# Performance work log

Hardware: AMD Instinct MI355X
Metric: run time of the kernel (lower is better)

The kernel has to match this reference:

```python
import jax, jax.numpy as jnp
import numpy as np

EMB_W, COMMIT_W, ENT_W = 1.0, 0.25, 0.1  # loss weights from init_kwargs


def setup_inputs() -> dict:
    key = jax.random.key(0)
    k1, k2 = jax.random.split(key)
    B, H, W, D, K = 32, 32, 32, 64, 1024
    inputs = jax.random.normal(k1, (B, H, W, D), dtype=jnp.float32)
    # keras RandomUniform default: U(-0.05, 0.05)
    codebook = jax.random.uniform(k2, (K, D), dtype=jnp.float32, minval=-0.05, maxval=0.05)
    return {"inputs": inputs, "codebook": codebook}


def reference(inputs, codebook):
    # inputs: [B,H,W,D], codebook: [K,D]
    D = inputs.shape[-1]
    x = inputs.reshape(-1, D)  # [N,D]
    dist = (
        jnp.sum(x * x, axis=-1, keepdims=True)
        - 2.0 * (x @ codebook.T)
        + jnp.sum(codebook * codebook, axis=-1)
    )  # [N,K]
    tokens = jnp.argmin(dist, axis=-1)  # [N]
    emb = codebook[tokens].reshape(inputs.shape)  # [B,H,W,D]

    embedding_loss = EMB_W * jnp.mean((jax.lax.stop_gradient(emb) - inputs) ** 2)
    commitment_loss = COMMIT_W * jnp.mean((emb - jax.lax.stop_gradient(inputs)) ** 2)
    # 'entropy' loss as written in call(): mean over codebook of per-code min distance
    entropy_loss = ENT_W * jnp.mean(jnp.min(dist, axis=0))
    loss = embedding_loss + commitment_loss + entropy_loss

    # training=True path: straight-through estimator
    out = inputs + jax.lax.stop_gradient(emb - inputs)
    return out, loss
```

## Files before the change

kernel.cpp:

```cpp
#include <hip/hip_runtime.h>
#include <math.h>

#define NROWS 32768
#define NCODE 1024
#define AMB_CAP 8192
#define GAP_THRESH 1.5e-4f

typedef __attribute__((ext_vector_type(8))) short bf16x8;
typedef __attribute__((ext_vector_type(4))) float f32x4;

__device__ __forceinline__ unsigned short bf16_rne(float f) {
    unsigned u = __float_as_uint(f);
    unsigned r = u + 0x7FFFu + ((u >> 16) & 1u);
    return (unsigned short)(r >> 16);
}

typedef const __attribute__((address_space(1))) unsigned GU;
typedef __attribute__((address_space(3))) unsigned LU;
__device__ __forceinline__ void gl_lds16(const void* g, void* l) {
    __builtin_amdgcn_global_load_lds((GU*)g, (LU*)l, 16, 0, 0);
}
__device__ __forceinline__ void gl_lds4(const void* g, void* l) {
    __builtin_amdgcn_global_load_lds((GU*)g, (LU*)l, 4, 0, 0);
}

__global__ __launch_bounds__(64) void vq_prep(
    const float* __restrict__ cb, float* __restrict__ cn4,
    unsigned* __restrict__ minK, unsigned* __restrict__ counter,
    float* __restrict__ gsumsq, unsigned* __restrict__ ticket,
    unsigned short* __restrict__ wsB)
{
    int c = blockIdx.x * 64 + threadIdx.x;
    if (c == 0) { *counter = 0u; *gsumsq = 0.f; *ticket = 0u; }
    float v[64];
    const float4* src = (const float4*)(cb + (size_t)c * 64);
    float s = 0.f;
    #pragma unroll
    for (int i = 0; i < 16; i++) {
        float4 t = src[i];
        v[i*4+0] = t.x; v[i*4+1] = t.y; v[i*4+2] = t.z; v[i*4+3] = t.w;
        s += t.x*t.x + t.y*t.y + t.z*t.z + t.w*t.w;
    }
    cn4[c] = s + 4.0f;
    minK[c] = 0x7F800000u;
    int cc = c >> 6, ct = (c >> 4) & 3, cl = c & 15;
    #pragma unroll
    for (int q = 0; q < 4; q++) {
        int half = q & 1, lo = q >> 1;
        #pragma unroll
        for (int g = 0; g < 4; g++) {
            unsigned short u8[8] __attribute__((aligned(16)));
            #pragma unroll
            for (int j = 0; j < 8; j++) {
                float f = v[half*32 + g*8 + j];
                unsigned short h = bf16_rne(f);
                if (lo) h = bf16_rne(f - __uint_as_float((unsigned)h << 16));
                u8[j] = h;
            }
            size_t off = (size_t)cc * 8192 + ct * 2048 + q * 512 + (g * 16 + cl) * 8;
            *(uint4*)(wsB + off) = *(const uint4*)u8;
        }
    }
}

__global__ __launch_bounds__(512, 4) void vq_main(
    const float* __restrict__ x, const float* __restrict__ cb,
    const unsigned short* __restrict__ wsB, const float* __restrict__ cn4,
    float* __restrict__ out, unsigned* __restrict__ minK,
    unsigned* __restrict__ counter, int* __restrict__ amb,
    float* __restrict__ gsumsq)
{
    __shared__ __align__(16) unsigned char Bb[2][16384];
    __shared__ float cn4L[2][64];
    __shared__ unsigned scrE[1024];
    __shared__ float mD1[128], mD2[128];
    __shared__ int   mI1[128];
    __shared__ int   tokS[64];
    __shared__ float redS[8];

    const int tid = threadIdx.x;
    const int lane = tid & 63;
    const int wi = tid >> 6;
    const int g = wi >> 1;
    const int h = wi & 1;
    const int ln15 = lane & 15;
    const int q = lane >> 4;
    const int row0 = blockIdx.x * 64;
    const int rot = blockIdx.x & 15;

    #pragma unroll
    for (int jj = 0; jj < 2; jj++) scrE[jj*512 + tid] = 0x7F800000u;

    const char* wsBb = (const char*)wsB;
    {
        int wbase = (tid & ~63) * 16;
        gl_lds16(wsBb + rot*16384 +        tid*16, (void*)&Bb[0][wbase]);
        gl_lds16(wsBb + rot*16384 + 8192 + tid*16, (void*)&Bb[0][8192 + wbase]);
        if (wi == 0) gl_lds4(cn4 + rot*64 + lane, (void*)&cn4L[0][0]);
    }

    bf16x8 Ah0, Ah1, Al0, Al1;
    float xnm4[4];
    {
        const float* xr = x + (size_t)(row0 + g*16 + ln15) * 64 + q * 8;
        float4 f0 = *(const float4*)xr;
        float4 f1 = *(const float4*)(xr + 4);
        float4 f2 = *(const float4*)(xr + 32);
        float4 f3 = *(const float4*)(xr + 36);
        float fa[8] = {f0.x,f0.y,f0.z,f0.w,f1.x,f1.y,f1.z,f1.w};
        float fb[8] = {f2.x,f2.y,f2.z,f2.w,f3.x,f3.y,f3.z,f3.w};
        unsigned short hh8[8] __attribute__((aligned(16)));
        unsigned short ll8[8] __attribute__((aligned(16)));
        unsigned short h28[8] __attribute__((aligned(16)));
        unsigned short l28[8] __attribute__((aligned(16)));
        float ss = 0.f;
        #pragma unroll
        for (int j = 0; j < 8; j++) {
            ss += fa[j]*fa[j] + fb[j]*fb[j];
            unsigned short hh = bf16_rne(fa[j]);
            hh8[j] = hh; ll8[j] = bf16_rne(fa[j] - __uint_as_float((unsigned)hh << 16));
            hh = bf16_rne(fb[j]);
            h28[j] = hh; l28[j] = bf16_rne(fb[j] - __uint_as_float((unsigned)hh << 16));
        }
        Ah0 = *(const bf16x8*)hh8; Al0 = *(const bf16x8*)ll8;
        Ah1 = *(const bf16x8*)h28; Al1 = *(const bf16x8*)l28;
        ss += __shfl_xor(ss, 16);
        ss += __shfl_xor(ss, 32);
        #pragma unroll
        for (int r = 0; r < 4; r++)
            xnm4[r] = __shfl(ss, (q << 2) | r, 64) - 4.0f;
    }

    float d1[4], d2[4];
    int   i1[4];
    #pragma unroll
    for (int r = 0; r < 4; r++) { d1[r] = INFINITY; d2[r] = INFINITY; i1[r] = 0; }

    for (int s = 0; s < 16; s++) {
        __syncthreads();
        const int cb_ = s & 1, nb = (s + 1) & 1;
        const int cphys = (s + rot) & 15;
        if (s < 15) {
            const int cnx = (s + 1 + rot) & 15;
            int wbase = (tid & ~63) * 16;
            gl_lds16(wsBb + cnx*16384 +        tid*16, (void*)&Bb[nb][wbase]);
            gl_lds16(wsBb + cnx*16384 + 8192 + tid*16, (void*)&Bb[nb][8192 + wbase]);
            if (wi == 0) gl_lds4(cn4 + cnx*64 + lane, (void*)&cn4L[nb][0]);
        }
        const unsigned char* buf = Bb[cb_];
        #pragma unroll
        for (int lct = 0; lct < 2; lct++) {
            const int ct = 2*h + lct;
            bf16x8 Bh0 = *(const bf16x8*)(buf + ct*4096 +    0 + lane*16);
            bf16x8 Bh1 = *(const bf16x8*)(buf + ct*4096 + 1024 + lane*16);
            bf16x8 Bl0 = *(const bf16x8*)(buf + ct*4096 + 2048 + lane*16);
            bf16x8 Bl1 = *(const bf16x8*)(buf + ct*4096 + 3072 + lane*16);
            float cn4v = cn4L[cb_][ct*16 + ln15];
            int kid = cphys*64 + ct*16 + ln15;
            f32x4 acc = {0.f, 0.f, 0.f, 0.f};
            acc = __builtin_amdgcn_mfma_f32_16x16x32_bf16(Ah0, Bh0, acc, 0, 0, 0);
            acc = __builtin_amdgcn_mfma_f32_16x16x32_bf16(Ah1, Bh1, acc, 0, 0, 0);
            acc = __builtin_amdgcn_mfma_f32_16x16x32_bf16(Ah0, Bl0, acc, 0, 0, 0);
            acc = __builtin_amdgcn_mfma_f32_16x16x32_bf16(Ah1, Bl1, acc, 0, 0, 0);
            acc = __builtin_amdgcn_mfma_f32_16x16x32_bf16(Al0, Bh0, acc, 0, 0, 0);
            acc = __builtin_amdgcn_mfma_f32_16x16x32_bf16(Al1, Bh1, acc, 0, 0, 0);
            float cminv = INFINITY;
            #pragma unroll
            for (int r = 0; r < 4; r++) {
                float wv = fmaf(acc[r], -2.0f, cn4v);
                bool lt = wv < d1[r];
                d2[r] = lt ? d1[r] : fminf(d2[r], wv);
                i1[r] = lt ? kid   : i1[r];
                d1[r] = lt ? wv    : d1[r];
                cminv = fminf(cminv, wv + xnm4[r]);
            }
            cminv = fminf(cminv, __shfl_xor(cminv, 16));
            cminv = fminf(cminv, __shfl_xor(cminv, 32));
            if (q == lct) atomicMin(&scrE[kid], __float_as_uint(cminv));
        }
    }
    __syncthreads();

    #pragma unroll
    for (int d = 1; d < 16; d <<= 1) {
        #pragma unroll
        for (int r = 0; r < 4; r++) {
            float od1 = __shfl_xor(d1[r], d);
            int   oi1 = __shfl_xor(i1[r], d);
            float od2 = __shfl_xor(d2[r], d);
            bool take = (od1 < d1[r]) || (od1 == d1[r] && oi1 < i1[r]);
            float loser = take ? d1[r] : od1;
            d2[r] = fminf(fminf(d2[r], od2), loser);
            d1[r] = take ? od1 : d1[r];
            i1[r] = take ? oi1 : i1[r];
        }
    }
    if (ln15 == 0) {
        #pragma unroll
        for (int r = 0; r < 4; r++) {
            int idx = (g*16 + q*4 + r) * 2 + h;
            mD1[idx] = d1[r]; mI1[idx] = i1[r]; mD2[idx] = d2[r];
        }
    }
    __syncthreads();

    if (tid < 64) {
        float a1 = mD1[tid*2],   b1 = mD1[tid*2+1];
        int   ai = mI1[tid*2],   bi = mI1[tid*2+1];
        float a2 = mD2[tid*2],   b2 = mD2[tid*2+1];
        bool ta = (a1 < b1) || (a1 == b1 && ai < bi);
        float D1 = ta ? a1 : b1;
        int   I1 = ta ? ai : bi;
        float D2 = ta ? fminf(a2, b1) : fminf(b2, a1);
        tokS[tid] = I1;
        if (D2 - D1 < GAP_THRESH) {
            unsigned idx = atomicAdd(counter, 1u);
            if (idx < AMB_CAP) { amb[2*idx] = row0 + tid; amb[2*idx+1] = I1; }
        }
    }

    #pragma unroll
    for (int jj = 0; jj < 2; jj++) {
        int c = jj*512 + tid;
        unsigned u = scrE[c];
        if (u < minK[c]) atomicMin(&minK[c], u);
    }
    __syncthreads();

    {
        float acc2 = 0.f;
        #pragma unroll
        for (int uu = 0; uu < 2; uu++) {
            int u = uu*512 + tid;
            int row = u >> 4, c4 = u & 15;
            int tok = tokS[row];
            float4 c = ((const float4*)(cb + (size_t)tok*64))[c4];
            float4 xx = ((const float4*)(x + (size_t)(row0 + row)*64))[c4];
            ((float4*)(out + (size_t)(row0 + row)*64))[c4] = c;
            float dx = c.x-xx.x, dy = c.y-xx.y, dz = c.z-xx.z, dw = c.w-xx.w;
            acc2 += dx*dx + dy*dy + dz*dz + dw*dw;
        }
        #pragma unroll
        for (int o = 32; o > 0; o >>= 1) acc2 += __shfl_down(acc2, o);
        if (lane == 0) redS[wi] = acc2;
        __syncthreads();
        if (tid == 0) {
            float t = 0.f;
            #pragma unroll
            for (int w = 0; w < 8; w++) t += redS[w];
            atomicAdd(gsumsq, t);
        }
    }
}

__global__ __launch_bounds__(256) void vq_tail(
    const float* __restrict__ x, const float* __restrict__ cb,
    float* __restrict__ out, const unsigned* __restrict__ counter,
    const int* __restrict__ amb, float* __restrict__ gsumsq,
    unsigned* __restrict__ ticket, const unsigned* __restrict__ minK,
    float* __restrict__ out_loss)
{
    __shared__ double xs[64];
    __shared__ double bd[256];
    __shared__ int    bi[256];
    __shared__ unsigned lastS;
    __shared__ float redS[4];

    const int tid = threadIdx.x;

    unsigned cnt = *counter; if (cnt > AMB_CAP) cnt = AMB_CAP;
    for (unsigned i = blockIdx.x; i < cnt; i += gridDim.x) {
        int row = amb[2*i], oldk = amb[2*i+1];
        __syncthreads();
        if (tid < 64) xs[tid] = (double)x[(size_t)row*64 + tid];
        __syncthreads();
        double xn = 0.0;
        #pragma unroll 8
        for (int d = 0; d < 64; d++) xn += xs[d]*xs[d];
        double best = INFINITY; int bk = 1 << 30;
        #pragma unroll
        for (int j = 0; j < 4; j++) {
            int k = j*256 + tid;
            const float4* c4 = (const float4*)(cb + (size_t)k*64);
            double dot = 0.0, cn2 = 0.0;
            #pragma unroll
            for (int t = 0; t < 16; t++) {
                float4 cv = c4[t];
                double cx = (double)cv.x, cy = (double)cv.y, cz = (double)cv.z, cw = (double)cv.w;
                dot += xs[t*4+0]*cx + xs[t*4+1]*cy + xs[t*4+2]*cz + xs[t*4+3]*cw;
                cn2 += cx*cx + cy*cy + cz*cz + cw*cw;
            }
            double dist = (xn - 2.0*dot) + cn2;
            if (dist < best || (dist == best && k < bk)) { best = dist; bk = k; }
        }
        bd[tid] = best; bi[tid] = bk;
        __syncthreads();
        for (int s = 128; s > 0; s >>= 1) {
            if (tid < s) {
                double od = bd[tid+s]; int ok = bi[tid+s];
                if (od < bd[tid] || (od == bd[tid] && ok < bi[tid])) { bd[tid] = od; bi[tid] = ok; }
            }
            __syncthreads();
        }
        int bestk = bi[0];
        if (bestk != oldk) {
            double part = 0.0;
            if (tid < 64) {
                float cn = cb[(size_t)bestk*64 + tid];
                float co = cb[(size_t)oldk*64 + tid];
                out[(size_t)row*64 + tid] = cn;
                double dn = (double)cn - xs[tid];
                double dl = (double)co - xs[tid];
                part = dn*dn - dl*dl;
            }
            __syncthreads();
            bd[tid] = part;
            __syncthreads();
            for (int s = 128; s > 0; s >>= 1) {
                if (tid < s) bd[tid] += bd[tid+s];
                __syncthreads();
            }
            if (tid == 0) atomicAdd(gsumsq, (float)bd[0]);
        }
    }

    __syncthreads();
    if (tid == 0) {
        __threadfence();
        lastS = (atomicAdd(ticket, 1u) == (unsigned)(gridDim.x - 1)) ? 1u : 0u;
    }
    __syncthreads();
    if (lastS) {
        __threadfence();
        float s = 0.f;
        #pragma unroll
        for (int jj = 0; jj < 4; jj++)
            s += __uint_as_float(minK[jj*256 + tid]);
        #pragma unroll
        for (int o = 32; o > 0; o >>= 1) s += __shfl_down(s, o);
        if ((tid & 63) == 0) redS[tid >> 6] = s;
        __syncthreads();
        if (tid == 0) {
            float gs = atomicAdd(gsumsq, 0.0f);
            float tot = redS[0] + redS[1] + redS[2] + redS[3];
            out_loss[0] = 1.25f * (gs / 2097152.0f) + 0.1f * (tot / 1024.0f);
        }
    }
}

extern "C" void kernel_launch(void* const* d_in, const int* in_sizes, int n_in,
                              void* d_out, int out_size, void* d_ws, size_t ws_size,
                              hipStream_t stream) {
    const float* x  = (const float*)d_in[0];
    const float* cb = (const float*)d_in[1];
    float* out = (float*)d_out;

    char* ws = (char*)d_ws;
    unsigned*       counter = (unsigned*)ws;
    float*          gsumsq  = (float*)(ws + 4);
    unsigned*       ticket  = (unsigned*)(ws + 8);
    float*          cn4     = (float*)(ws + 1024);
    unsigned*       minK    = (unsigned*)(ws + 8192);
    int*            amb     = (int*)(ws + 16384);
    unsigned short* wsB     = (unsigned short*)(ws + 131072);

    vq_prep<<<16,  64,  0, stream>>>(cb, cn4, minK, counter, gsumsq, ticket, wsB);
    vq_main<<<512, 512, 0, stream>>>(x, cb, wsB, cn4, out, minK, counter, amb, gsumsq);
    vq_tail<<<64,  256, 0, stream>>>(x, cb, out, counter, amb, gsumsq, ticket, minK,
                                     out + 2097152);
}
```

Baseline: 130.6 us.

## Halve rows per block, give each wave one code tile, split MFMA chains

Each block now handles 32 rows instead of 64, and each of the 8 waves takes a single 16-code tile in place of two. This doubles the grid to 1024 blocks and raises the occupancy hint to 8 blocks. The six dependent MFMAs are split into two independent accumulator chains that are summed afterwards, shortening the dependency chain. In exchange, every block still streams the whole codebook through LDS, so total codebook traffic and per-block minK atomics double. The final argmin merge now reduces across 4 code quarters.

```diff
diff --git a/kernel.cpp b/kernel.cpp
--- a/kernel.cpp
+++ b/kernel.cpp
@@ -63,7 +63,7 @@
     }
 }
 
-__global__ __launch_bounds__(512, 4) void vq_main(
+__global__ __launch_bounds__(512, 8) void vq_main(
     const float* __restrict__ x, const float* __restrict__ cb,
     const unsigned short* __restrict__ wsB, const float* __restrict__ cn4,
     float* __restrict__ out, unsigned* __restrict__ minK,
@@ -75,21 +75,21 @@
     __shared__ unsigned scrE[1024];
     __shared__ float mD1[128], mD2[128];
     __shared__ int   mI1[128];
-    __shared__ int   tokS[64];
+    __shared__ int   tokS[32];
     __shared__ float redS[8];
 
     const int tid = threadIdx.x;
     const int lane = tid & 63;
     const int wi = tid >> 6;
-    const int g = wi >> 1;
-    const int h = wi & 1;
+    const int g = wi >> 2;
+    const int cq = wi & 3;
     const int ln15 = lane & 15;
     const int q = lane >> 4;
-    const int row0 = blockIdx.x * 64;
+    const int row0 = blockIdx.x * 32;
     const int rot = blockIdx.x & 15;
 
-    #pragma unroll
-    for (int jj = 0; jj < 2; jj++) scrE[jj*512 + tid] = 0x7F800000u;
+    scrE[tid] = 0x7F800000u;
+    scrE[512 + tid] = 0x7F800000u;
 
     const char* wsBb = (const char*)wsB;
     {
@@ -148,26 +148,26 @@
             if (wi == 0) gl_lds4(cn4 + cnx*64 + lane, (void*)&cn4L[nb][0]);
         }
         const unsigned char* buf = Bb[cb_];
-        #pragma unroll
-        for (int lct = 0; lct < 2; lct++) {
-            const int ct = 2*h + lct;
+        {
+            const int ct = cq;
             bf16x8 Bh0 = *(const bf16x8*)(buf + ct*4096 +    0 + lane*16);
             bf16x8 Bh1 = *(const bf16x8*)(buf + ct*4096 + 1024 + lane*16);
             bf16x8 Bl0 = *(const bf16x8*)(buf + ct*4096 + 2048 + lane*16);
             bf16x8 Bl1 = *(const bf16x8*)(buf + ct*4096 + 3072 + lane*16);
             float cn4v = cn4L[cb_][ct*16 + ln15];
             int kid = cphys*64 + ct*16 + ln15;
-            f32x4 acc = {0.f, 0.f, 0.f, 0.f};
-            acc = __builtin_amdgcn_mfma_f32_16x16x32_bf16(Ah0, Bh0, acc, 0, 0, 0);
-            acc = __builtin_amdgcn_mfma_f32_16x16x32_bf16(Ah1, Bh1, acc, 0, 0, 0);
-            acc = __builtin_amdgcn_mfma_f32_16x16x32_bf16(Ah0, Bl0, acc, 0, 0, 0);
-            acc = __builtin_amdgcn_mfma_f32_16x16x32_bf16(Ah1, Bl1, acc, 0, 0, 0);
-            acc = __builtin_amdgcn_mfma_f32_16x16x32_bf16(Al0, Bh0, acc, 0, 0, 0);
-            acc = __builtin_amdgcn_mfma_f32_16x16x32_bf16(Al1, Bh1, acc, 0, 0, 0);
+            f32x4 z = {0.f, 0.f, 0.f, 0.f};
+            f32x4 acc0 = __builtin_amdgcn_mfma_f32_16x16x32_bf16(Ah0, Bh0, z, 0, 0, 0);
+            f32x4 acc1 = __builtin_amdgcn_mfma_f32_16x16x32_bf16(Ah1, Bh1, z, 0, 0, 0);
+            acc0 = __builtin_amdgcn_mfma_f32_16x16x32_bf16(Ah0, Bl0, acc0, 0, 0, 0);
+            acc1 = __builtin_amdgcn_mfma_f32_16x16x32_bf16(Ah1, Bl1, acc1, 0, 0, 0);
+            acc0 = __builtin_amdgcn_mfma_f32_16x16x32_bf16(Al0, Bh0, acc0, 0, 0, 0);
+            acc1 = __builtin_amdgcn_mfma_f32_16x16x32_bf16(Al1, Bh1, acc1, 0, 0, 0);
             float cminv = INFINITY;
             #pragma unroll
             for (int r = 0; r < 4; r++) {
-                float wv = fmaf(acc[r], -2.0f, cn4v);
+                float sdot = acc0[r] + acc1[r];
+                float wv = fmaf(sdot, -2.0f, cn4v);
                 bool lt = wv < d1[r];
                 d2[r] = lt ? d1[r] : fminf(d2[r], wv);
                 i1[r] = lt ? kid   : i1[r];
@@ -176,7 +176,7 @@
             }
             cminv = fminf(cminv, __shfl_xor(cminv, 16));
             cminv = fminf(cminv, __shfl_xor(cminv, 32));
-            if (q == lct) atomicMin(&scrE[kid], __float_as_uint(cminv));
+            if (q == 0) atomicMin(&scrE[kid], __float_as_uint(cminv));
         }
     }
     __syncthreads();
@@ -198,20 +198,23 @@
     if (ln15 == 0) {
         #pragma unroll
         for (int r = 0; r < 4; r++) {
-            int idx = (g*16 + q*4 + r) * 2 + h;
+            int idx = (g*16 + q*4 + r) * 4 + cq;
             mD1[idx] = d1[r]; mI1[idx] = i1[r]; mD2[idx] = d2[r];
         }
     }
     __syncthreads();
 
-    if (tid < 64) {
-        float a1 = mD1[tid*2],   b1 = mD1[tid*2+1];
-        int   ai = mI1[tid*2],   bi = mI1[tid*2+1];
-        float a2 = mD2[tid*2],   b2 = mD2[tid*2+1];
-        bool ta = (a1 < b1) || (a1 == b1 && ai < bi);
-        float D1 = ta ? a1 : b1;
-        int   I1 = ta ? ai : bi;
-        float D2 = ta ? fminf(a2, b1) : fminf(b2, a1);
+    if (tid < 32) {
+        float D1 = mD1[tid*4], D2 = mD2[tid*4];
+        int   I1 = mI1[tid*4];
+        #pragma unroll
+        for (int c = 1; c < 4; c++) {
+            float b1 = mD1[tid*4+c], b2 = mD2[tid*4+c];
+            int   bi = mI1[tid*4+c];
+            bool tb = (b1 < D1) || (b1 == D1 && bi < I1);
+            if (tb) { D2 = fminf(D1, b2); D1 = b1; I1 = bi; }
+            else    { D2 = fminf(D2, b1); }
+        }
         tokS[tid] = I1;
         if (D2 - D1 < GAP_THRESH) {
             unsigned idx = atomicAdd(counter, 1u);
@@ -219,27 +222,22 @@
         }
     }
 
-    #pragma unroll
-    for (int jj = 0; jj < 2; jj++) {
-        int c = jj*512 + tid;
-        unsigned u = scrE[c];
-        if (u < minK[c]) atomicMin(&minK[c], u);
-    }
-    __syncthreads();
-
     {
-        float acc2 = 0.f;
-        #pragma unroll
-        for (int uu = 0; uu < 2; uu++) {
-            int u = uu*512 + tid;
-            int row = u >> 4, c4 = u & 15;
-            int tok = tokS[row];
-            float4 c = ((const float4*)(cb + (size_t)tok*64))[c4];
-            float4 xx = ((const float4*)(x + (size_t)(row0 + row)*64))[c4];
-            ((float4*)(out + (size_t)(row0 + row)*64))[c4] = c;
-            float dx = c.x-xx.x, dy = c.y-xx.y, dz = c.z-xx.z, dw = c.w-xx.w;
-            acc2 += dx*dx + dy*dy + dz*dz + dw*dw;
-        }
+        unsigned u0 = scrE[tid];
+        if (u0 < minK[tid]) atomicMin(&minK[tid], u0);
+        unsigned u1 = scrE[512 + tid];
+        if (u1 < minK[512 + tid]) atomicMin(&minK[512 + tid], u1);
+    }
+    __syncthreads();
+
+    {
+        int row = tid >> 4, c4 = tid & 15;
+        int tok = tokS[row];
+        float4 c = ((const float4*)(cb + (size_t)tok*64))[c4];
+        float4 xx = ((const float4*)(x + (size_t)(row0 + row)*64))[c4];
+        ((float4*)(out + (size_t)(row0 + row)*64))[c4] = c;
+        float dx = c.x-xx.x, dy = c.y-xx.y, dz = c.z-xx.z, dw = c.w-xx.w;
+        float acc2 = dx*dx + dy*dy + dz*dz + dw*dw;
         #pragma unroll
         for (int o = 32; o > 0; o >>= 1) acc2 += __shfl_down(acc2, o);
         if (lane == 0) redS[wi] = acc2;
@@ -364,8 +362,8 @@
     int*            amb     = (int*)(ws + 16384);
     unsigned short* wsB     = (unsigned short*)(ws + 131072);
 
-    vq_prep<<<16,  64,  0, stream>>>(cb, cn4, minK, counter, gsumsq, ticket, wsB);
-    vq_main<<<512, 512, 0, stream>>>(x, cb, wsB, cn4, out, minK, counter, amb, gsumsq);
-    vq_tail<<<64,  256, 0, stream>>>(x, cb, out, counter, amb, gsumsq, ticket, minK,
-                                     out + 2097152);
-}
+    vq_prep<<<16,   64,  0, stream>>>(cb, cn4, minK, counter, gsumsq, ticket, wsB);
+    vq_main<<<1024, 512, 0, stream>>>(x, cb, wsB, cn4, out, minK, counter, amb, gsumsq);
+    vq_tail<<<64,   256, 0, stream>>>(x, cb, out, counter, amb, gsumsq, ticket, minK,
+                                      out + 2097152);
+}
```

After: 203.3 us. 55.7% more time.
